# Optimization experiments

Hardware: AMD Instinct MI355X
Metric: run time of the kernel (lower is better)

Reference implementation:

```python
import jax, jax.numpy as jnp
import numpy as np

N_NODES = 100000
K_HOPS = 10
ALPHA = 0.1


def gcn_conv(x, src, dst, W, b, num_nodes):
    # GCNConv: linear first (cheaper: out_dim small), then D^-1/2 (A+I) D^-1/2 aggregation
    h = x @ W  # [N, out]
    deg = jax.ops.segment_sum(jnp.ones_like(dst, dtype=h.dtype), dst, num_segments=num_nodes)
    dinv = jnp.where(deg > 0, jax.lax.rsqrt(deg), 0.0)
    norm = dinv[src] * dinv[dst]  # [E]
    msg = h[src] * norm[:, None]
    out = jax.ops.segment_sum(msg, dst, num_segments=num_nodes)
    return out + b


def _with_self_loops(edge_index, num_nodes):
    loops = jnp.arange(num_nodes, dtype=edge_index.dtype)
    src = jnp.concatenate([edge_index[0], loops])
    dst = jnp.concatenate([edge_index[1], loops])
    return src, dst


def setup_inputs() -> dict:
    key = jax.random.key(0)
    ks = jax.random.split(key, 8)
    n_feat, hidden, n_cls, n_edges = 512, 16, 7, 3200000
    x = jax.random.normal(ks[0], (N_NODES, n_feat), dtype=jnp.float32)
    edge_index = jax.random.randint(ks[1], (2, n_edges), 0, N_NODES, dtype=jnp.int64)
    W1 = jax.random.normal(ks[2], (n_feat, hidden), dtype=jnp.float32) * 0.05
    b1 = jnp.zeros((hidden,), dtype=jnp.float32)
    Wl = jax.random.normal(ks[3], (hidden, hidden), dtype=jnp.float32) * 0.25
    bl = jnp.zeros((hidden,), dtype=jnp.float32)
    W2 = jax.random.normal(ks[4], (hidden, n_cls), dtype=jnp.float32) * 0.25
    b2 = jnp.zeros((n_cls,), dtype=jnp.float32)
    return {"x": x, "edge_index": edge_index, "W1": W1, "b1": b1, "Wl": Wl, "bl": bl, "W2": W2, "b2": b2}


def reference(x, edge_index, W1, b1, Wl, bl, W2, b2):
    src, dst = _with_self_loops(edge_index, N_NODES)
    h = jax.nn.relu(gcn_conv(x, src, dst, W1, b1, N_NODES))
    def body(h, _):
        h = ALPHA * jax.nn.relu(h @ Wl + bl) + (1.0 - ALPHA) * h
        return h, None
    h, _ = jax.lax.scan(body, h, None, length=K_HOPS)
    out = gcn_conv(h, src, dst, W2, b2, N_NODES)
    return jax.nn.log_softmax(out, axis=1)
```

## Files before the change

kernel.cpp:

```cpp
#include <hip/hip_runtime.h>
#include <math.h>

#define N_NODES 100000
#define N_EDGES 3200000
#define F_IN    512
#define HID     16
#define NCLS    7
#define ALPHA   0.1f
#define K_HOPS  10

#define SHIFT   7
#define BWIDTH  128
#define NBUCK   ((N_NODES + BWIDTH - 1) / BWIDTH)
#define CHUNK   16384
#define A3_BLOCKS ((N_EDGES + CHUNK - 1) / CHUNK)

#define OFF_BCNT    0u
#define OFF_BSTART  1024u
#define OFF_BCUR    2048u
#define OFF_RP      3072u
#define OFF_DINV    103424u
#define OFF_COL     203776u
#define OFF_BINNED  3403776u
#define OFF_H0      3403776u
#define OFF_H1      5003776u
#define OFF_Z       6603776u

__global__ void k_bhist(const int* __restrict__ dst, int* __restrict__ bcnt) {
    __shared__ int h[NBUCK];
    int tid = threadIdx.x;
    for (int i = tid; i < NBUCK; i += 256) h[i] = 0;
    __syncthreads();
    for (int e = blockIdx.x * 256 + tid; e < N_EDGES; e += gridDim.x * 256)
        atomicAdd(&h[dst[e] >> SHIFT], 1);
    __syncthreads();
    for (int i = tid; i < NBUCK; i += 256) {
        int v = h[i];
        if (v) atomicAdd(&bcnt[i], v);
    }
}

__global__ void k_bscan(const int* __restrict__ bcnt, int* __restrict__ bstart,
                        int* __restrict__ bcur) {
    __shared__ int s[1024];
    int tid = threadIdx.x;
    int v = (tid < NBUCK) ? bcnt[tid] : 0;
    s[tid] = v;
    __syncthreads();
    for (int off = 1; off < 1024; off <<= 1) {
        int t = (tid >= off) ? s[tid - off] : 0;
        __syncthreads();
        s[tid] += t;
        __syncthreads();
    }
    if (tid < NBUCK) {
        int ex = s[tid] - v;
        bstart[tid] = ex;
        bcur[tid] = ex;
    }
    if (tid == 0) bstart[NBUCK] = N_EDGES;
}

__global__ void k_bin(const int* __restrict__ src, const int* __restrict__ dst,
                      int* __restrict__ bcur, unsigned int* __restrict__ binned) {
    __shared__ int ha[1024];
    __shared__ int hb[1024];
    __shared__ int gbase[NBUCK];
    __shared__ int lcur[NBUCK];
    int tid = threadIdx.x;
    int e0 = blockIdx.x * CHUNK;
    int e1 = e0 + CHUNK;
    if (e1 > N_EDGES) e1 = N_EDGES;
    for (int i = tid; i < 1024; i += 256) ha[i] = 0;
    __syncthreads();
    for (int e = e0 + tid; e < e1; e += 256)
        atomicAdd(&ha[dst[e] >> SHIFT], 1);
    __syncthreads();
    int* a = ha;
    int* b = hb;
    for (int off = 1; off < 1024; off <<= 1) {
        for (int s = tid; s < 1024; s += 256)
            b[s] = a[s] + ((s >= off) ? a[s - off] : 0);
        __syncthreads();
        int* t = a; a = b; b = t;
    }
    for (int s = tid; s < NBUCK; s += 256) {
        int c = a[s] - ((s > 0) ? a[s - 1] : 0);
        lcur[s] = 0;
        gbase[s] = c ? atomicAdd(&bcur[s], c) : 0;
    }
    __syncthreads();
    for (int e = e0 + tid; e < e1; e += 256) {
        int d = dst[e];
        int bk = d >> SHIFT;
        int idx = atomicAdd(&lcur[bk], 1);
        binned[gbase[bk] + idx] =
            ((unsigned int)(d & (BWIDTH - 1)) << 17) | (unsigned int)src[e];
    }
}

__global__ void k_csr(const unsigned int* __restrict__ binned, const int* __restrict__ bstart,
                      int* __restrict__ rp, float* __restrict__ dinv, int* __restrict__ col) {
    __shared__ int cnt[BWIDTH];
    __shared__ int s[BWIDTH];
    __shared__ int cur[BWIDTH];
    int tid = threadIdx.x;
    int b = blockIdx.x;
    int base = b << SHIFT;
    int e0 = bstart[b], e1 = bstart[b + 1];
    if (tid < BWIDTH) cnt[tid] = 0;
    __syncthreads();
    for (int e = e0 + tid; e < e1; e += 256)
        atomicAdd(&cnt[binned[e] >> 17], 1);
    __syncthreads();
    int v = 0;
    if (tid < BWIDTH) { v = cnt[tid]; s[tid] = v; }
    __syncthreads();
    for (int off = 1; off < BWIDTH; off <<= 1) {
        int t = 0;
        if (tid < BWIDTH && tid >= off) t = s[tid - off];
        __syncthreads();
        if (tid < BWIDTH) s[tid] += t;
        __syncthreads();
    }
    if (tid < BWIDTH) {
        int ex = s[tid] - v;
        cur[tid] = ex;
        int node = base + tid;
        if (node < N_NODES) {
            rp[node] = e0 + ex;
            dinv[node] = rsqrtf((float)(v + 1));
        }
    }
    if (b == 0 && tid == 0) rp[N_NODES] = N_EDGES;
    __syncthreads();
    for (int e = e0 + tid; e < e1; e += 256) {
        unsigned int w = binned[e];
        int ln = (int)(w >> 17);
        int p = atomicAdd(&cur[ln], 1);
        col[e0 + p] = (int)(w & 0x1FFFFu);
    }
}

__global__ void k_xw1(const float* __restrict__ x, const float* __restrict__ W,
                      float* __restrict__ h0) {
    int row = blockIdx.x * blockDim.x + threadIdx.x;
    if (row >= N_NODES) return;
    const float4* x4 = (const float4*)(x + (size_t)row * F_IN);
    float acc[HID];
#pragma unroll
    for (int c = 0; c < HID; c++) acc[c] = 0.f;
    for (int k4 = 0; k4 < F_IN / 4; k4++) {
        float4 xv = x4[k4];
        int k = k4 * 4;
#pragma unroll
        for (int j = 0; j < 4; j++) {
            float xj = (j == 0) ? xv.x : (j == 1) ? xv.y : (j == 2) ? xv.z : xv.w;
#pragma unroll
            for (int c = 0; c < HID; c++)
                acc[c] += xj * W[(k + j) * HID + c];
        }
    }
    float4* o4 = (float4*)(h0 + (size_t)row * HID);
#pragma unroll
    for (int q = 0; q < HID / 4; q++) {
        float4 v;
        v.x = acc[q * 4 + 0]; v.y = acc[q * 4 + 1];
        v.z = acc[q * 4 + 2]; v.w = acc[q * 4 + 3];
        o4[q] = v;
    }
}

__global__ void k_agg1(const float* __restrict__ h0, const int* __restrict__ rp,
                       const int* __restrict__ col, const float* __restrict__ dinv,
                       const float* __restrict__ b1, float* __restrict__ h1) {
    int t = blockIdx.x * blockDim.x + threadIdx.x;
    int node = t >> 4;
    int c = t & 15;
    if (node >= N_NODES) return;
    float dv = dinv[node];
    float acc = dv * h0[(size_t)node * HID + c];
    int e0 = rp[node], e1 = rp[node + 1];
    for (int e = e0; e < e1; e++) {
        int s = col[e];
        acc += dinv[s] * h0[(size_t)s * HID + c];
    }
    float o = dv * acc + b1[c];
    h1[(size_t)node * HID + c] = fmaxf(o, 0.f);
}

__global__ void k_hops(const float* __restrict__ h1, const float* __restrict__ Wl,
                       const float* __restrict__ bl, const float* __restrict__ W2,
                       float* __restrict__ z) {
    int node = blockIdx.x * blockDim.x + threadIdx.x;
    if (node >= N_NODES) return;
    float h[HID];
    const float4* h4 = (const float4*)(h1 + (size_t)node * HID);
#pragma unroll
    for (int q = 0; q < HID / 4; q++) {
        float4 v = h4[q];
        h[q * 4 + 0] = v.x; h[q * 4 + 1] = v.y;
        h[q * 4 + 2] = v.z; h[q * 4 + 3] = v.w;
    }
    for (int it = 0; it < K_HOPS; it++) {
        float tm[HID];
#pragma unroll
        for (int c = 0; c < HID; c++) tm[c] = bl[c];
#pragma unroll
        for (int k = 0; k < HID; k++) {
            float hk = h[k];
#pragma unroll
            for (int c = 0; c < HID; c++) tm[c] += hk * Wl[k * HID + c];
        }
#pragma unroll
        for (int c = 0; c < HID; c++)
            h[c] = ALPHA * fmaxf(tm[c], 0.f) + (1.f - ALPHA) * h[c];
    }
    float zz[8];
#pragma unroll
    for (int c = 0; c < 8; c++) zz[c] = 0.f;
#pragma unroll
    for (int k = 0; k < HID; k++) {
        float hk = h[k];
#pragma unroll
        for (int c = 0; c < NCLS; c++) zz[c] += hk * W2[k * NCLS + c];
    }
    float4* z4 = (float4*)(z + (size_t)node * 8);
    float4 v0, v1;
    v0.x = zz[0]; v0.y = zz[1]; v0.z = zz[2]; v0.w = zz[3];
    v1.x = zz[4]; v1.y = zz[5]; v1.z = zz[6]; v1.w = zz[7];
    z4[0] = v0; z4[1] = v1;
}

__global__ void k_agg2(const float* __restrict__ z, const int* __restrict__ rp,
                       const int* __restrict__ col, const float* __restrict__ dinv,
                       const float* __restrict__ b2, float* __restrict__ out) {
    int t = blockIdx.x * blockDim.x + threadIdx.x;
    int node = t >> 3;
    int c = t & 7;
    if (node >= N_NODES) return;
    float dv = dinv[node];
    float acc = dv * z[(size_t)node * 8 + c];
    int e0 = rp[node], e1 = rp[node + 1];
    for (int e = e0; e < e1; e++) {
        int s = col[e];
        acc += dinv[s] * z[(size_t)s * 8 + c];
    }
    float o = dv * acc + ((c < NCLS) ? b2[c] : 0.f);
    float val = (c < NCLS) ? o : -INFINITY;
    float m = val;
    m = fmaxf(m, __shfl_xor(m, 1));
    m = fmaxf(m, __shfl_xor(m, 2));
    m = fmaxf(m, __shfl_xor(m, 4));
    float ex = (c < NCLS) ? expf(o - m) : 0.f;
    float ss = ex;
    ss += __shfl_xor(ss, 1);
    ss += __shfl_xor(ss, 2);
    ss += __shfl_xor(ss, 4);
    if (c < NCLS) out[(size_t)node * NCLS + c] = o - m - logf(ss);
}

extern "C" void kernel_launch(void* const* d_in, const int* in_sizes, int n_in,
                              void* d_out, int out_size, void* d_ws, size_t ws_size,
                              hipStream_t stream) {
    const float* x  = (const float*)d_in[0];
    const int*   ei = (const int*)d_in[1];
    const float* W1 = (const float*)d_in[2];
    const float* b1 = (const float*)d_in[3];
    const float* Wl = (const float*)d_in[4];
    const float* bl = (const float*)d_in[5];
    const float* W2 = (const float*)d_in[6];
    const float* b2 = (const float*)d_in[7];
    float* out = (float*)d_out;

    int*   wsI = (int*)d_ws;
    float* wsF = (float*)d_ws;
    int*          bcnt   = wsI + OFF_BCNT;
    int*          bstart = wsI + OFF_BSTART;
    int*          bcur   = wsI + OFF_BCUR;
    int*          rp     = wsI + OFF_RP;
    float*        dinv   = wsF + OFF_DINV;
    int*          col    = wsI + OFF_COL;
    unsigned int* binned = (unsigned int*)(wsI + OFF_BINNED);
    float*        h0     = wsF + OFF_H0;
    float*        h1     = wsF + OFF_H1;
    float*        z      = wsF + OFF_Z;

    const int* src = ei;
    const int* dst = ei + N_EDGES;

    hipMemsetAsync(bcnt, 0, NBUCK * sizeof(int), stream);

    k_bhist<<<512, 256, 0, stream>>>(dst, bcnt);
    k_bscan<<<1, 1024, 0, stream>>>(bcnt, bstart, bcur);
    k_bin<<<A3_BLOCKS, 256, 0, stream>>>(src, dst, bcur, binned);
    k_csr<<<NBUCK, 256, 0, stream>>>(binned, bstart, rp, dinv, col);
    k_xw1<<<(N_NODES + 255) / 256, 256, 0, stream>>>(x, W1, h0);
    k_agg1<<<(N_NODES * 16 + 255) / 256, 256, 0, stream>>>(h0, rp, col, dinv, b1, h1);
    k_hops<<<(N_NODES + 255) / 256, 256, 0, stream>>>(h1, Wl, bl, W2, z);
    k_agg2<<<(N_NODES * 8 + 255) / 256, 256, 0, stream>>>(z, rp, col, dinv, b2, out);
}
```

Baseline: 649.3 us.

## Prescale features by dinv, split-K the input GEMM, unroll gathers, retune edge binning

Source-side dinv scaling is folded into the producer kernels (xw1 and hops), so the aggregation loops no longer gather dinv[s] per edge. The x@W1 kernel now splits the 512-wide reduction across four wavefronts per block and reduces the partial sums through shared memory, which gives more parallelism over 64 rows per block. Both gather loops are unrolled by two to keep more loads in flight. The binning chunk size and histogram grid size are also retuned. All of this adds shared memory and a block-wide sync to the GEMM kernel.

```diff
diff --git a/kernel.cpp b/kernel.cpp
--- a/kernel.cpp
+++ b/kernel.cpp
@@ -12,7 +12,7 @@
 #define SHIFT   7
 #define BWIDTH  128
 #define NBUCK   ((N_NODES + BWIDTH - 1) / BWIDTH)
-#define CHUNK   16384
+#define CHUNK   8192
 #define A3_BLOCKS ((N_EDGES + CHUNK - 1) / CHUNK)
 
 #define OFF_BCNT    0u
@@ -142,56 +142,71 @@
     }
 }
 
+#define XW_ROWS 64
 __global__ void k_xw1(const float* __restrict__ x, const float* __restrict__ W,
-                      float* __restrict__ h0) {
-    int row = blockIdx.x * blockDim.x + threadIdx.x;
-    if (row >= N_NODES) return;
-    const float4* x4 = (const float4*)(x + (size_t)row * F_IN);
+                      const float* __restrict__ dinv, float* __restrict__ h0s) {
+    __shared__ float red[4][XW_ROWS][HID + 1];
+    int lane = threadIdx.x & 63;
+    int sp   = threadIdx.x >> 6;
+    int rowBase = blockIdx.x * XW_ROWS;
+    int row = rowBase + lane;
     float acc[HID];
 #pragma unroll
     for (int c = 0; c < HID; c++) acc[c] = 0.f;
-    for (int k4 = 0; k4 < F_IN / 4; k4++) {
-        float4 xv = x4[k4];
-        int k = k4 * 4;
-#pragma unroll
-        for (int j = 0; j < 4; j++) {
-            float xj = (j == 0) ? xv.x : (j == 1) ? xv.y : (j == 2) ? xv.z : xv.w;
-#pragma unroll
-            for (int c = 0; c < HID; c++)
-                acc[c] += xj * W[(k + j) * HID + c];
+    if (row < N_NODES) {
+        const float4* x4 = (const float4*)(x + (size_t)row * F_IN + sp * (F_IN / 4));
+        for (int k4 = 0; k4 < F_IN / 16; k4++) {
+            float4 xv = x4[k4];
+            int kb = sp * (F_IN / 4) + k4 * 4;
+#pragma unroll
+            for (int j = 0; j < 4; j++) {
+                float xj = (j == 0) ? xv.x : (j == 1) ? xv.y : (j == 2) ? xv.z : xv.w;
+#pragma unroll
+                for (int c = 0; c < HID; c++)
+                    acc[c] += xj * W[(kb + j) * HID + c];
+            }
         }
     }
-    float4* o4 = (float4*)(h0 + (size_t)row * HID);
-#pragma unroll
-    for (int q = 0; q < HID / 4; q++) {
-        float4 v;
-        v.x = acc[q * 4 + 0]; v.y = acc[q * 4 + 1];
-        v.z = acc[q * 4 + 2]; v.w = acc[q * 4 + 3];
-        o4[q] = v;
-    }
-}
-
-__global__ void k_agg1(const float* __restrict__ h0, const int* __restrict__ rp,
+#pragma unroll
+    for (int c = 0; c < HID; c++) red[sp][lane][c] = acc[c];
+    __syncthreads();
+#pragma unroll
+    for (int p = 0; p < 4; p++) {
+        int f = threadIdx.x + p * 256;
+        int r = f >> 4, c = f & 15;
+        int node = rowBase + r;
+        if (node < N_NODES) {
+            float v = red[0][r][c] + red[1][r][c] + red[2][r][c] + red[3][r][c];
+            h0s[(size_t)node * HID + c] = dinv[node] * v;
+        }
+    }
+}
+
+__global__ void k_agg1(const float* __restrict__ h0s, const int* __restrict__ rp,
                        const int* __restrict__ col, const float* __restrict__ dinv,
                        const float* __restrict__ b1, float* __restrict__ h1) {
     int t = blockIdx.x * blockDim.x + threadIdx.x;
     int node = t >> 4;
     int c = t & 15;
     if (node >= N_NODES) return;
-    float dv = dinv[node];
-    float acc = dv * h0[(size_t)node * HID + c];
+    float acc = h0s[(size_t)node * HID + c];
     int e0 = rp[node], e1 = rp[node + 1];
-    for (int e = e0; e < e1; e++) {
-        int s = col[e];
-        acc += dinv[s] * h0[(size_t)s * HID + c];
-    }
-    float o = dv * acc + b1[c];
+    int e = e0;
+    for (; e + 1 < e1; e += 2) {
+        int s0 = col[e], s1 = col[e + 1];
+        float v0 = h0s[(size_t)s0 * HID + c];
+        float v1 = h0s[(size_t)s1 * HID + c];
+        acc += v0;
+        acc += v1;
+    }
+    if (e < e1) acc += h0s[(size_t)col[e] * HID + c];
+    float o = dinv[node] * acc + b1[c];
     h1[(size_t)node * HID + c] = fmaxf(o, 0.f);
 }
 
 __global__ void k_hops(const float* __restrict__ h1, const float* __restrict__ Wl,
                        const float* __restrict__ bl, const float* __restrict__ W2,
-                       float* __restrict__ z) {
+                       const float* __restrict__ dinv, float* __restrict__ zs) {
     int node = blockIdx.x * blockDim.x + threadIdx.x;
     if (node >= N_NODES) return;
     float h[HID];
@@ -216,6 +231,7 @@
         for (int c = 0; c < HID; c++)
             h[c] = ALPHA * fmaxf(tm[c], 0.f) + (1.f - ALPHA) * h[c];
     }
+    float dv = dinv[node];
     float zz[8];
 #pragma unroll
     for (int c = 0; c < 8; c++) zz[c] = 0.f;
@@ -225,28 +241,32 @@
 #pragma unroll
         for (int c = 0; c < NCLS; c++) zz[c] += hk * W2[k * NCLS + c];
     }
-    float4* z4 = (float4*)(z + (size_t)node * 8);
+    float4* z4 = (float4*)(zs + (size_t)node * 8);
     float4 v0, v1;
-    v0.x = zz[0]; v0.y = zz[1]; v0.z = zz[2]; v0.w = zz[3];
-    v1.x = zz[4]; v1.y = zz[5]; v1.z = zz[6]; v1.w = zz[7];
+    v0.x = dv * zz[0]; v0.y = dv * zz[1]; v0.z = dv * zz[2]; v0.w = dv * zz[3];
+    v1.x = dv * zz[4]; v1.y = dv * zz[5]; v1.z = dv * zz[6]; v1.w = 0.f;
     z4[0] = v0; z4[1] = v1;
 }
 
-__global__ void k_agg2(const float* __restrict__ z, const int* __restrict__ rp,
+__global__ void k_agg2(const float* __restrict__ zs, const int* __restrict__ rp,
                        const int* __restrict__ col, const float* __restrict__ dinv,
                        const float* __restrict__ b2, float* __restrict__ out) {
     int t = blockIdx.x * blockDim.x + threadIdx.x;
     int node = t >> 3;
     int c = t & 7;
     if (node >= N_NODES) return;
-    float dv = dinv[node];
-    float acc = dv * z[(size_t)node * 8 + c];
+    float acc = zs[(size_t)node * 8 + c];
     int e0 = rp[node], e1 = rp[node + 1];
-    for (int e = e0; e < e1; e++) {
-        int s = col[e];
-        acc += dinv[s] * z[(size_t)s * 8 + c];
-    }
-    float o = dv * acc + ((c < NCLS) ? b2[c] : 0.f);
+    int e = e0;
+    for (; e + 1 < e1; e += 2) {
+        int s0 = col[e], s1 = col[e + 1];
+        float v0 = zs[(size_t)s0 * 8 + c];
+        float v1 = zs[(size_t)s1 * 8 + c];
+        acc += v0;
+        acc += v1;
+    }
+    if (e < e1) acc += zs[(size_t)col[e] * 8 + c];
+    float o = dinv[node] * acc + ((c < NCLS) ? b2[c] : 0.f);
     float val = (c < NCLS) ? o : -INFINITY;
     float m = val;
     m = fmaxf(m, __shfl_xor(m, 1));
@@ -282,21 +302,21 @@
     float*        dinv   = wsF + OFF_DINV;
     int*          col    = wsI + OFF_COL;
     unsigned int* binned = (unsigned int*)(wsI + OFF_BINNED);
-    float*        h0     = wsF + OFF_H0;
+    float*        h0s    = wsF + OFF_H0;
     float*        h1     = wsF + OFF_H1;
-    float*        z      = wsF + OFF_Z;
+    float*        zs     = wsF + OFF_Z;
 
     const int* src = ei;
     const int* dst = ei + N_EDGES;
 
     hipMemsetAsync(bcnt, 0, NBUCK * sizeof(int), stream);
 
-    k_bhist<<<512, 256, 0, stream>>>(dst, bcnt);
+    k_bhist<<<1024, 256, 0, stream>>>(dst, bcnt);
     k_bscan<<<1, 1024, 0, stream>>>(bcnt, bstart, bcur);
     k_bin<<<A3_BLOCKS, 256, 0, stream>>>(src, dst, bcur, binned);
     k_csr<<<NBUCK, 256, 0, stream>>>(binned, bstart, rp, dinv, col);
-    k_xw1<<<(N_NODES + 255) / 256, 256, 0, stream>>>(x, W1, h0);
-    k_agg1<<<(N_NODES * 16 + 255) / 256, 256, 0, stream>>>(h0, rp, col, dinv, b1, h1);
-    k_hops<<<(N_NODES + 255) / 256, 256, 0, stream>>>(h1, Wl, bl, W2, z);
-    k_agg2<<<(N_NODES * 8 + 255) / 256, 256, 0, stream>>>(z, rp, col, dinv, b2, out);
-}
+    k_xw1<<<(N_NODES + XW_ROWS - 1) / XW_ROWS, 256, 0, stream>>>(x, W1, dinv, h0s);
+    k_agg1<<<(N_NODES * 16 + 255) / 256, 256, 0, stream>>>(h0s, rp, col, dinv, b1, h1);
+    k_hops<<<(N_NODES + 255) / 256, 256, 0, stream>>>(h1, Wl, bl, W2, dinv, zs);
+    k_agg2<<<(N_NODES * 8 + 255) / 256, 256, 0, stream>>>(zs, rp, col, dinv, b2, out);
+}
```

New measurement: 643.6 us. About the same (-0.9%).
